# Optimization experiments

Hardware: AMD Instinct MI355X
Metric: run time of the kernel (lower is better)

## Reference

```python
import jax, jax.numpy as jnp
import numpy as np

EPS = 1e-5

def _lin_bn_relu(x, W, b, gamma, beta):
    # x: [N, Cin], W: [Cout, Cin] (torch layout), b/gamma/beta: [Cout]
    y = x @ W.T + b
    mu = jnp.mean(y, axis=0)                      # training-mode batch stats
    var = jnp.mean((y - mu) ** 2, axis=0)         # biased variance (torch BN)
    yhat = (y - mu) * jax.lax.rsqrt(var + EPS)
    return jax.nn.relu(gamma * yhat + beta)


def setup_inputs() -> dict:
    key = jax.random.key(0)
    ks = jax.random.split(key, 16)
    N = 262144
    dims = [(64, 3), (512, 64), (512, 512), (2, 512)]
    inp = {
        "x1": jax.random.normal(ks[0], (8, 4, 8, 8), dtype=jnp.float32),
        "x2": jax.random.normal(ks[1], (N, 3), dtype=jnp.float32),
    }
    for i, (co, ci) in enumerate(dims, start=1):
        lim = 1.0 / np.sqrt(ci)
        inp[f"W{i}"] = jax.random.uniform(ks[2 * i], (co, ci), jnp.float32, -lim, lim)
        inp[f"b{i}"] = jax.random.uniform(ks[2 * i + 1], (co,), jnp.float32, -lim, lim)
    for i, c in enumerate([64, 512, 512], start=1):
        inp[f"gamma{i}"] = jnp.ones((c,), jnp.float32)
        inp[f"beta{i}"] = jnp.zeros((c,), jnp.float32)
    return inp


def reference(x1, x2, W1, b1, W2, b2, W3, b3, W4, b4,
              gamma1, beta1, gamma2, beta2, gamma3, beta3):
    # x1 is sliced in the original forward (x[0][:, 0:-1]) but unused in the output.
    h = _lin_bn_relu(x2, W1, b1, gamma1, beta1)   # [N, 64]
    h = _lin_bn_relu(h, W2, b2, gamma2, beta2)    # [N, 512]
    h = _lin_bn_relu(h, W3, b3, gamma3, beta3)    # [N, 512]
    out = h @ W4.T + b4                           # [N, 2]
    return out
```

## Files before the change

### kernel.cpp

```cpp
#include <hip/hip_runtime.h>

typedef __bf16 bf16x4 __attribute__((ext_vector_type(4)));
typedef __bf16 bf16x8 __attribute__((ext_vector_type(8)));
typedef float f32x4 __attribute__((ext_vector_type(4)));

#define MFMA_BF16 __builtin_amdgcn_mfma_f32_16x16x32_bf16

__global__ __launch_bounds__(256) void prep_kernel(
    const float* __restrict__ W2, const float* __restrict__ W3,
    __bf16* __restrict__ W2bf, __bf16* __restrict__ W3bf,
    float* __restrict__ stats) {
  int i = blockIdx.x * 256 + threadIdx.x;
  if (i < 32768) W2bf[i] = (__bf16)W2[i];
  if (i < 262144) W3bf[i] = (__bf16)W3[i];
  if (i < 5312) stats[i] = 0.f;
}

__global__ __launch_bounds__(256) void stats1_kernel(
    const float* __restrict__ x, const float* __restrict__ W1,
    const float* __restrict__ b1, float* __restrict__ gsum,
    float* __restrict__ gsq) {
  int t = threadIdx.x;
  int c = t & 63;
  int rw = t >> 6;
  float w0 = W1[c * 3 + 0], w1 = W1[c * 3 + 1], w2 = W1[c * 3 + 2];
  float b = b1[c];
  int base = blockIdx.x * 128;
  float sum = 0.f, sq = 0.f;
#pragma unroll 4
  for (int i = 0; i < 32; ++i) {
    int row = base + i * 4 + rw;
    const float* xp = x + (size_t)row * 3;
    float y = fmaf(xp[0], w0, fmaf(xp[1], w1, fmaf(xp[2], w2, b)));
    sum += y;
    sq += y * y;
  }
  __shared__ float ssum[256], ssq[256];
  ssum[t] = sum;
  ssq[t] = sq;
  __syncthreads();
  if (t < 64) {
    float s = ssum[t] + ssum[t + 64] + ssum[t + 128] + ssum[t + 192];
    float q = ssq[t] + ssq[t + 64] + ssq[t + 128] + ssq[t + 192];
    atomicAdd(&gsum[t], s);
    atomicAdd(&gsq[t], q);
  }
}

__global__ void finalize1_kernel(const float* __restrict__ gsum,
                                 const float* __restrict__ gsq,
                                 const float* __restrict__ gamma,
                                 const float* __restrict__ beta,
                                 const float* __restrict__ W1,
                                 const float* __restrict__ b1,
                                 float* __restrict__ fold1, float invN) {
  int c = threadIdx.x;
  float mu = gsum[c] * invN;
  float var = gsq[c] * invN - mu * mu;
  float sc = gamma[c] * rsqrtf(var + 1e-5f);
  float sh = beta[c] - mu * sc;
  fold1[c] = sc * W1[c * 3 + 0];
  fold1[64 + c] = sc * W1[c * 3 + 1];
  fold1[128 + c] = sc * W1[c * 3 + 2];
  fold1[192 + c] = sc * b1[c] + sh;
}

__global__ void finalize3_kernel(const float* __restrict__ gsum,
                                 const float* __restrict__ gsq,
                                 const float* __restrict__ gamma,
                                 const float* __restrict__ beta,
                                 const float* __restrict__ b,
                                 float* __restrict__ scale,
                                 float* __restrict__ shiftf,
                                 float* __restrict__ shiftp, float invN) {
  int c = blockIdx.x * blockDim.x + threadIdx.x;
  if (c >= 512) return;
  float mu = gsum[c] * invN;
  float var = gsq[c] * invN - mu * mu;
  float sc = gamma[c] * rsqrtf(var + 1e-5f);
  float sh = beta[c] - mu * sc;
  scale[c] = sc;
  shiftf[c] = sc * b[c] + sh;
  shiftp[c] = sh;
}

__global__ __launch_bounds__(256, 4) void m1_kernel(
    const float* __restrict__ x2, const float* __restrict__ fold1,
    float* __restrict__ M1, float* __restrict__ s1) {
  __shared__ float sF[256];
  __shared__ float xs[768];
  __shared__ __bf16 h1T[64 * 264];
  __shared__ float s1s[4][64];

  const int t = threadIdx.x;
  const int lane = t & 63, wave = t >> 6;
  const int lrow = lane & 15, lgrp = lane >> 4;

  sF[t] = fold1[t];
  if (t < 192)
    ((float4*)xs)[t] = ((const float4*)(x2 + (size_t)blockIdx.x * 768))[t];
  __syncthreads();

  const int c0 = (t & 3) * 16;
  const int r0 = t >> 2;
  float sAcc[16] = {};
#pragma unroll
  for (int s = 0; s < 4; ++s) {
    int r = r0 + s * 64;
    float X0 = xs[r * 3], X1 = xs[r * 3 + 1], X2 = xs[r * 3 + 2];
#pragma unroll
    for (int j = 0; j < 16; ++j) {
      int c = c0 + j;
      float h = fmaxf(
          fmaf(sF[c], X0, fmaf(sF[64 + c], X1, fmaf(sF[128 + c], X2, sF[192 + c]))),
          0.f);
      sAcc[j] += h;
      h1T[c * 264 + r] = (__bf16)h;
    }
  }
  __syncthreads();

  f32x4 acc[4] = {};
#pragma unroll
  for (int kk = 0; kk < 256; kk += 32) {
    bf16x8 af = *(const bf16x8*)&h1T[(wave * 16 + lrow) * 264 + kk + lgrp * 8];
#pragma unroll
    for (int n = 0; n < 4; ++n) {
      bf16x8 bfr = *(const bf16x8*)&h1T[(n * 16 + lrow) * 264 + kk + lgrp * 8];
      acc[n] = MFMA_BF16(af, bfr, acc[n], 0, 0, 0);
    }
  }
#pragma unroll
  for (int n = 0; n < 4; ++n)
#pragma unroll
    for (int rr = 0; rr < 4; ++rr)
      atomicAdd(&M1[(wave * 16 + lgrp * 4 + rr) * 64 + n * 16 + lrow],
                acc[n][rr]);

#pragma unroll
  for (int j = 0; j < 16; ++j) {
    float v = sAcc[j];
    v += __shfl_xor(v, 4);
    v += __shfl_xor(v, 8);
    v += __shfl_xor(v, 16);
    v += __shfl_xor(v, 32);
    if (lane < 4) s1s[wave][(lane & 3) * 16 + j] = v;
  }
  __syncthreads();
  if (t < 64)
    atomicAdd(&s1[t], s1s[0][t] + s1s[1][t] + s1s[2][t] + s1s[3][t]);
}

__global__ __launch_bounds__(256) void finalize2v_kernel(
    const float* __restrict__ M1, const float* __restrict__ s1,
    const float* __restrict__ W2, const float* __restrict__ b2,
    const float* __restrict__ gamma2, const float* __restrict__ beta2,
    float* __restrict__ scale2, float* __restrict__ shift2f, float fN) {
  __shared__ float sM[64 * 65];
  __shared__ float ss[64];
  int t = threadIdx.x;
  for (int i = t; i < 4096; i += 256) sM[(i >> 6) * 65 + (i & 63)] = M1[i];
  if (t < 64) ss[t] = s1[t];
  __syncthreads();
  int lane = t & 63;
  int col = blockIdx.x * 4 + (t >> 6);
  float wi = W2[(size_t)col * 64 + lane];
  float p = 0.f;
#pragma unroll
  for (int j = 0; j < 64; ++j) p = fmaf(sM[lane * 65 + j], __shfl(wi, j), p);
  float qi = wi * p;
  float swi = ss[lane] * wi;
#pragma unroll
  for (int off = 1; off < 64; off <<= 1) {
    qi += __shfl_xor(qi, off);
    swi += __shfl_xor(swi, off);
  }
  if (lane == 0) {
    float b = b2[col];
    float sy = swi + fN * b;
    float sqs = qi + 2.f * b * swi + fN * b * b;
    float mu = sy / fN;
    float var = sqs / fN - mu * mu;
    float sc = gamma2[col] * rsqrtf(var + 1e-5f);
    scale2[col] = sc;
    shift2f[col] = (beta2[col] - mu * sc) + sc * b;
  }
}

#define G3_LD(BUF, K)                                                        \
  _Pragma("unroll") for (int m = 0; m < 4; ++m) BUF[m] =                     \
      *(const bf16x8*)&h2r[(m * 16 + lrow) * 520 + (K) * 32 + lgrp * 8];

#define G3_MM(BUF, K)                                                        \
  __builtin_amdgcn_s_setprio(1);                                             \
  _Pragma("unroll") for (int m = 0; m < 4; ++m) {                            \
    acc[m][0] = MFMA_BF16(BUF[m], b3r[K][0], acc[m][0], 0, 0, 0);            \
    acc[m][1] = MFMA_BF16(BUF[m], b3r[K][1], acc[m][1], 0, 0, 0);            \
  }                                                                          \
  __builtin_amdgcn_s_setprio(0);

template <int MODE>
__global__ __launch_bounds__(512, 2) void fused_kernel(
    const float* __restrict__ x2, const float* __restrict__ fold1,
    const __bf16* __restrict__ W2bf, const float* __restrict__ scale2,
    const float* __restrict__ shift2f, const __bf16* __restrict__ W3bf,
    const float* __restrict__ b3, const float* __restrict__ scale3,
    const float* __restrict__ shift3f, const float* __restrict__ W4,
    const float* __restrict__ b4, float* __restrict__ gsum3,
    float* __restrict__ gsq3, float* __restrict__ out,
    __bf16* __restrict__ y3o, int gBase, int gCount, int rStoreRgs) {
  __shared__ __bf16 h1buf[2][64 * 72];
  __shared__ __bf16 h2buf[2][64 * 520];
  __shared__ float sF[256];
  __shared__ float sSc2[512], sSh2[512];
  __shared__ float outaccW[8][64][2];

  const int t = threadIdx.x;
  const int lane = t & 63, wave = t >> 6;
  const int lrow = lane & 15, lgrp = lane >> 4;
  const int colHalf = blockIdx.x & 1;
  const int rgFirst = gBase + (int)(blockIdx.x >> 1) * gCount;
  const int wCol3 = colHalf * 256 + wave * 32;
  const int wCol2 = wave * 64;
  const bool doStore = (MODE == 3) && (rgFirst < rStoreRgs);

  if (t < 256) sF[t] = fold1[t];
  sSc2[t] = scale2[t & 511];
  sSh2[t] = shift2f[t & 511];

  bf16x8 b2r[2][4];
#pragma unroll
  for (int kk = 0; kk < 2; ++kk)
#pragma unroll
    for (int n = 0; n < 4; ++n)
      b2r[kk][n] = *(const bf16x8*)&W2bf[(wCol2 + n * 16 + lrow) * 64 +
                                         kk * 32 + lgrp * 8];
  bf16x8 b3r[16][2];
#pragma unroll
  for (int k = 0; k < 16; ++k)
#pragma unroll
    for (int n = 0; n < 2; ++n)
      b3r[k][n] = *(const bf16x8*)&W3bf[(size_t)(wCol3 + n * 16 + lrow) * 512 +
                                        k * 32 + lgrp * 8];

  const int c3a = wCol3 + lrow, c3b = wCol3 + 16 + lrow;
  float b3a = 0.f, b3b = 0.f;
  float sc3a = 0.f, sc3b = 0.f, sh3a = 0.f, sh3b = 0.f;
  float w40a = 0.f, w40b = 0.f, w41a = 0.f, w41b = 0.f, B40 = 0.f, B41 = 0.f;
  if (MODE != 2) {
    b3a = b3[c3a];
    b3b = b3[c3b];
  } else {
    sc3a = scale3[c3a];
    sc3b = scale3[c3b];
    sh3a = shift3f[c3a];
    sh3b = shift3f[c3b];
    w40a = W4[c3a];
    w40b = W4[c3b];
    w41a = W4[512 + c3a];
    w41b = W4[512 + c3b];
    B40 = b4[0];
    B41 = b4[1];
  }
  float csA = 0.f, cqA = 0.f, csB = 0.f, cqB = 0.f;

  const int hr = t >> 3, hc0 = (t & 7) * 8;
  const float* xbase = x2 + ((size_t)rgFirst * 64 + hr) * 3;
  float xa, xb, xc;

  auto stageH1 = [&](__bf16* h1p) {
    bf16x8 hv;
#pragma unroll
    for (int j = 0; j < 8; ++j) {
      int c = hc0 + j;
      float h = fmaf(sF[c], xa,
                     fmaf(sF[64 + c], xb, fmaf(sF[128 + c], xc, sF[192 + c])));
      hv[j] = (__bf16)fmaxf(h, 0.f);
    }
    *(bf16x8*)&h1p[hr * 72 + hc0] = hv;
  };

  auto gemm2 = [&](const __bf16* h1p, __bf16* h2p) {
#pragma unroll
    for (int nh = 0; nh < 2; ++nh) {
      f32x4 a2[2][4] = {};
#pragma unroll
      for (int kk = 0; kk < 2; ++kk) {
        bf16x8 af0 = *(const bf16x8*)&h1p[(0 * 16 + lrow) * 72 + kk * 32 + lgrp * 8];
        bf16x8 af1 = *(const bf16x8*)&h1p[(1 * 16 + lrow) * 72 + kk * 32 + lgrp * 8];
        bf16x8 af2 = *(const bf16x8*)&h1p[(2 * 16 + lrow) * 72 + kk * 32 + lgrp * 8];
        bf16x8 af3 = *(const bf16x8*)&h1p[(3 * 16 + lrow) * 72 + kk * 32 + lgrp * 8];
#pragma unroll
        for (int n2 = 0; n2 < 2; ++n2) {
          int n = nh * 2 + n2;
          a2[n2][0] = MFMA_BF16(b2r[kk][n], af0, a2[n2][0], 0, 0, 0);
          a2[n2][1] = MFMA_BF16(b2r[kk][n], af1, a2[n2][1], 0, 0, 0);
          a2[n2][2] = MFMA_BF16(b2r[kk][n], af2, a2[n2][2], 0, 0, 0);
          a2[n2][3] = MFMA_BF16(b2r[kk][n], af3, a2[n2][3], 0, 0, 0);
        }
      }
#pragma unroll
      for (int n2 = 0; n2 < 2; ++n2) {
        int ch0 = wCol2 + (nh * 2 + n2) * 16 + lgrp * 4;
        float s0 = sSc2[ch0], s1v = sSc2[ch0 + 1], s2v = sSc2[ch0 + 2],
              s3v = sSc2[ch0 + 3];
        float z0 = sSh2[ch0], z1 = sSh2[ch0 + 1], z2 = sSh2[ch0 + 2],
              z3 = sSh2[ch0 + 3];
#pragma unroll
        for (int m = 0; m < 4; ++m) {
          int row = m * 16 + lrow;
          bf16x4 hv;
          hv[0] = (__bf16)fmaxf(fmaf(s0, a2[n2][m][0], z0), 0.f);
          hv[1] = (__bf16)fmaxf(fmaf(s1v, a2[n2][m][1], z1), 0.f);
          hv[2] = (__bf16)fmaxf(fmaf(s2v, a2[n2][m][2], z2), 0.f);
          hv[3] = (__bf16)fmaxf(fmaf(s3v, a2[n2][m][3], z3), 0.f);
          *(bf16x4*)&h2p[row * 520 + ch0] = hv;
        }
      }
    }
  };

  __syncthreads();

  xa = xbase[0];
  xb = xbase[1];
  xc = xbase[2];
  stageH1(h1buf[0]);
  __syncthreads();
  gemm2(h1buf[0], h2buf[0]);
  if (gCount > 1) {
    const float* xn = xbase + 192;
    xa = xn[0];
    xb = xn[1];
    xc = xn[2];
    stageH1(h1buf[1]);
  }
  __syncthreads();

  for (int g = 0; g < gCount; ++g) {
    const int rBase = (rgFirst + g) * 64;
    const __bf16* h2r = h2buf[g & 1];

    if (g + 2 < gCount) {
      const float* xn = xbase + (size_t)(g + 2) * 192;
      xa = xn[0];
      xb = xn[1];
      xc = xn[2];
    }

    if (g + 1 < gCount) gemm2(h1buf[(g + 1) & 1], h2buf[(g + 1) & 1]);

    if (g + 2 < gCount) stageH1(h1buf[g & 1]);

    f32x4 acc[4][2] = {};
    bf16x8 afA[4], afB[4];
    G3_LD(afA, 0)
#pragma unroll
    for (int k = 0; k < 16; k += 2) {
      G3_LD(afB, k + 1)
      G3_MM(afA, k)
      if (k < 14) { G3_LD(afA, k + 2) }
      G3_MM(afB, k + 1)
    }

    if (MODE != 2) {
#pragma unroll
      for (int m = 0; m < 4; ++m)
#pragma unroll
        for (int rr = 0; rr < 4; ++rr) {
          float ya = acc[m][0][rr] + b3a;
          float yb = acc[m][1][rr] + b3b;
          csA += ya;
          cqA = fmaf(ya, ya, cqA);
          csB += yb;
          cqB = fmaf(yb, yb, cqB);
          if (doStore) {
            size_t row = (size_t)(rBase + m * 16 + lgrp * 4 + rr);
            y3o[row * 512 + c3a] = (__bf16)ya;
            y3o[row * 512 + c3b] = (__bf16)yb;
          }
        }
    } else {
#pragma unroll
      for (int m = 0; m < 4; ++m)
#pragma unroll
        for (int rr = 0; rr < 4; ++rr) {
          float ha = fmaxf(fmaf(sc3a, acc[m][0][rr], sh3a), 0.f);
          float hb = fmaxf(fmaf(sc3b, acc[m][1][rr], sh3b), 0.f);
          float dd0 = fmaf(ha, w40a, hb * w40b);
          float dd1 = fmaf(ha, w41a, hb * w41b);
          dd0 += __shfl_xor(dd0, 1);
          dd1 += __shfl_xor(dd1, 1);
          dd0 += __shfl_xor(dd0, 2);
          dd1 += __shfl_xor(dd1, 2);
          dd0 += __shfl_xor(dd0, 4);
          dd1 += __shfl_xor(dd1, 4);
          dd0 += __shfl_xor(dd0, 8);
          dd1 += __shfl_xor(dd1, 8);
          if (lrow == 0) {
            int row = m * 16 + lgrp * 4 + rr;
            outaccW[wave][row][0] = dd0;
            outaccW[wave][row][1] = dd1;
          }
        }
    }
    __syncthreads();
  }

  if (MODE != 2) {
    csA += __shfl_xor(csA, 16);
    cqA += __shfl_xor(cqA, 16);
    csB += __shfl_xor(csB, 16);
    cqB += __shfl_xor(cqB, 16);
    csA += __shfl_xor(csA, 32);
    cqA += __shfl_xor(cqA, 32);
    csB += __shfl_xor(csB, 32);
    cqB += __shfl_xor(cqB, 32);
    if (lgrp == 0) {
      atomicAdd(&gsum3[c3a], csA);
      atomicAdd(&gsq3[c3a], cqA);
      atomicAdd(&gsum3[c3b], csB);
      atomicAdd(&gsq3[c3b], cqB);
    }
  } else {
    if (t < 128) {
      int row = t >> 1, o = t & 1;
      float s = 0.f;
#pragma unroll
      for (int w = 0; w < 8; ++w) s += outaccW[w][row][o];
      if (colHalf == 0) s += (o == 0) ? B40 : B41;
      atomicAdd(&out[(size_t)(rgFirst * 64 + row) * 2 + o], s);
    }
  }
}

__global__ __launch_bounds__(256) void stream_out_kernel(
    const __bf16* __restrict__ y3, const float* __restrict__ scale3,
    const float* __restrict__ shift3p, const float* __restrict__ W4,
    const float* __restrict__ b4, float* __restrict__ out, int N) {
  __shared__ float sSc[512], sSh[512], sW0[512], sW1[512];
  int t = threadIdx.x;
  for (int i = t; i < 512; i += 256) {
    sSc[i] = scale3[i];
    sSh[i] = shift3p[i];
    sW0[i] = W4[i];
    sW1[i] = W4[512 + i];
  }
  __syncthreads();
  int lane = t & 63, wv = t >> 6;
  int c0 = lane * 8;
  float fsc[8], fsh[8], fw0[8], fw1[8];
#pragma unroll
  for (int j = 0; j < 8; ++j) {
    fsc[j] = sSc[c0 + j];
    fsh[j] = sSh[c0 + j];
    fw0[j] = sW0[c0 + j];
    fw1[j] = sW1[c0 + j];
  }
  float B0 = b4[0], B1 = b4[1];
  for (size_t row = (size_t)blockIdx.x * 4 + wv; row < (size_t)N;
       row += (size_t)gridDim.x * 4) {
    bf16x8 v = *(const bf16x8*)(y3 + row * 512 + c0);
    float d0 = 0.f, d1 = 0.f;
#pragma unroll
    for (int j = 0; j < 8; ++j) {
      float h = fmaxf(fmaf(fsc[j], (float)v[j], fsh[j]), 0.f);
      d0 = fmaf(h, fw0[j], d0);
      d1 = fmaf(h, fw1[j], d1);
    }
#pragma unroll
    for (int off = 1; off < 64; off <<= 1) {
      d0 += __shfl_xor(d0, off);
      d1 += __shfl_xor(d1, off);
    }
    if (lane == 0) {
      out[row * 2 + 0] = d0 + B0;
      out[row * 2 + 1] = d1 + B1;
    }
  }
}

extern "C" void kernel_launch(void* const* d_in, const int* in_sizes, int n_in,
                              void* d_out, int out_size, void* d_ws,
                              size_t ws_size, hipStream_t stream) {
  const float* x2 = (const float*)d_in[1];
  const float* W1 = (const float*)d_in[2];
  const float* b1 = (const float*)d_in[3];
  const float* W2 = (const float*)d_in[4];
  const float* b2 = (const float*)d_in[5];
  const float* W3 = (const float*)d_in[6];
  const float* b3 = (const float*)d_in[7];
  const float* W4 = (const float*)d_in[8];
  const float* b4 = (const float*)d_in[9];
  const float* gamma1 = (const float*)d_in[10];
  const float* beta1 = (const float*)d_in[11];
  const float* gamma2 = (const float*)d_in[12];
  const float* beta2 = (const float*)d_in[13];
  const float* gamma3 = (const float*)d_in[14];
  const float* beta3 = (const float*)d_in[15];
  float* out = (float*)d_out;

  const int N = in_sizes[1] / 3;
  const float invN = 1.0f / (float)N;

  float* f0 = (float*)d_ws;
  float* gsum1 = f0;
  float* gsq1 = f0 + 64;
  float* M1 = f0 + 128;
  float* s1 = f0 + 4224;
  float* gsum3 = f0 + 4288;
  float* gsq3 = f0 + 4800;
  float* fold1 = f0 + 5312;
  float* scale2 = f0 + 5568;
  float* shift2f = f0 + 6080;
  float* scale3 = f0 + 6592;
  float* shift3f = f0 + 7104;
  float* shift3p = f0 + 7616;
  __bf16* W2bf = (__bf16*)(f0 + 8128);
  __bf16* W3bf = W2bf + 32768;

  const size_t y3off = (size_t)1 << 20;
  size_t availRows = (ws_size > y3off) ? (ws_size - y3off) / 1024 : 0;
  int rStoreBlks = (int)((availRows / 1024 < (size_t)(N / 1024))
                             ? availRows / 1024
                             : (size_t)(N / 1024));
  const int rStore = rStoreBlks * 1024;
  __bf16* y3bf = (__bf16*)((char*)d_ws + y3off);

  prep_kernel<<<1024, 256, 0, stream>>>(W2, W3, W2bf, W3bf, f0);
  stats1_kernel<<<N / 128, 256, 0, stream>>>(x2, W1, b1, gsum1, gsq1);
  finalize1_kernel<<<1, 64, 0, stream>>>(gsum1, gsq1, gamma1, beta1, W1, b1,
                                         fold1, invN);
  m1_kernel<<<N / 256, 256, 0, stream>>>(x2, fold1, M1, s1);
  finalize2v_kernel<<<128, 256, 0, stream>>>(M1, s1, W2, b2, gamma2, beta2,
                                             scale2, shift2f, (float)N);

  fused_kernel<3><<<(N / 1024) * 2, 512, 0, stream>>>(
      x2, fold1, W2bf, scale2, shift2f, W3bf, b3, scale3, shift3f, W4, b4,
      gsum3, gsq3, out, y3bf, 0, 16, rStoreBlks * 16);
  finalize3_kernel<<<1, 512, 0, stream>>>(gsum3, gsq3, gamma3, beta3, b3,
                                          scale3, shift3f, shift3p, invN);

  if (rStore > 0)
    stream_out_kernel<<<2048, 256, 0, stream>>>(y3bf, scale3, shift3p, W4, b4,
                                                out, rStore);
  if (rStore < N) {
    hipMemsetAsync(out + (size_t)rStore * 2, 0,
                   (size_t)(N - rStore) * 2 * sizeof(float), stream);
    fused_kernel<2><<<((N - rStore) / 64) * 2, 512, 0, stream>>>(
        x2, fold1, W2bf, scale2, shift2f, W3bf, b3, scale3, shift3f, W4, b4,
        gsum3, gsq3, out, y3bf, rStore / 64, 1, 0);
  }
}
```

Baseline: 389.8 us.

## Fold finalize kernels into consumers, merge prep with stats1, pair rows in stream_out

Removes the finalize1 and finalize3 launches by having each consumer kernel recompute the BN scale and shift from the raw sums in its prologue. Weight conversion to bf16 moves into extra blocks of the stats1 kernel using vectorized loads, and zeroing the stats buffer becomes a memset. The stream_out kernel now handles two rows per wave and shares the cross-lane reduction between four partial sums. The aim is fewer kernel launches and less shuffle work, at the cost of redundant per-block prologue math.

After: 384.1 us. Within noise of the previous version (-1.5%).

```diff
diff --git a/kernel.cpp b/kernel.cpp
--- a/kernel.cpp
+++ b/kernel.cpp
@@ -6,32 +6,52 @@
 
 #define MFMA_BF16 __builtin_amdgcn_mfma_f32_16x16x32_bf16
 
-__global__ __launch_bounds__(256) void prep_kernel(
-    const float* __restrict__ W2, const float* __restrict__ W3,
-    __bf16* __restrict__ W2bf, __bf16* __restrict__ W3bf,
-    float* __restrict__ stats) {
-  int i = blockIdx.x * 256 + threadIdx.x;
-  if (i < 32768) W2bf[i] = (__bf16)W2[i];
-  if (i < 262144) W3bf[i] = (__bf16)W3[i];
-  if (i < 5312) stats[i] = 0.f;
-}
-
-__global__ __launch_bounds__(256) void stats1_kernel(
+__global__ __launch_bounds__(256) void prep_stats1_kernel(
     const float* __restrict__ x, const float* __restrict__ W1,
-    const float* __restrict__ b1, float* __restrict__ gsum,
+    const float* __restrict__ b1, const float* __restrict__ W2,
+    const float* __restrict__ W3, __bf16* __restrict__ W2bf,
+    __bf16* __restrict__ W3bf, float* __restrict__ gsum,
     float* __restrict__ gsq) {
-  int t = threadIdx.x;
+  const int b = blockIdx.x;
+  const int t = threadIdx.x;
+  if (b >= 2048) {
+    const float* src;
+    __bf16* dst;
+    int idx;
+    if (b < 2064) {
+      idx = (b - 2048) * 2048 + t * 8;
+      src = W2;
+      dst = W2bf;
+    } else {
+      idx = (b - 2064) * 2048 + t * 8;
+      src = W3;
+      dst = W3bf;
+    }
+    float4 f0 = *(const float4*)(src + idx);
+    float4 f1 = *(const float4*)(src + idx + 4);
+    bf16x8 o;
+    o[0] = (__bf16)f0.x;
+    o[1] = (__bf16)f0.y;
+    o[2] = (__bf16)f0.z;
+    o[3] = (__bf16)f0.w;
+    o[4] = (__bf16)f1.x;
+    o[5] = (__bf16)f1.y;
+    o[6] = (__bf16)f1.z;
+    o[7] = (__bf16)f1.w;
+    *(bf16x8*)(dst + idx) = o;
+    return;
+  }
   int c = t & 63;
   int rw = t >> 6;
   float w0 = W1[c * 3 + 0], w1 = W1[c * 3 + 1], w2 = W1[c * 3 + 2];
-  float b = b1[c];
-  int base = blockIdx.x * 128;
+  float bb = b1[c];
+  int base = b * 128;
   float sum = 0.f, sq = 0.f;
 #pragma unroll 4
   for (int i = 0; i < 32; ++i) {
     int row = base + i * 4 + rw;
     const float* xp = x + (size_t)row * 3;
-    float y = fmaf(xp[0], w0, fmaf(xp[1], w1, fmaf(xp[2], w2, b)));
+    float y = fmaf(xp[0], w0, fmaf(xp[1], w1, fmaf(xp[2], w2, bb)));
     sum += y;
     sq += y * y;
   }
@@ -47,46 +67,12 @@
   }
 }
 
-__global__ void finalize1_kernel(const float* __restrict__ gsum,
-                                 const float* __restrict__ gsq,
-                                 const float* __restrict__ gamma,
-                                 const float* __restrict__ beta,
-                                 const float* __restrict__ W1,
-                                 const float* __restrict__ b1,
-                                 float* __restrict__ fold1, float invN) {
-  int c = threadIdx.x;
-  float mu = gsum[c] * invN;
-  float var = gsq[c] * invN - mu * mu;
-  float sc = gamma[c] * rsqrtf(var + 1e-5f);
-  float sh = beta[c] - mu * sc;
-  fold1[c] = sc * W1[c * 3 + 0];
-  fold1[64 + c] = sc * W1[c * 3 + 1];
-  fold1[128 + c] = sc * W1[c * 3 + 2];
-  fold1[192 + c] = sc * b1[c] + sh;
-}
-
-__global__ void finalize3_kernel(const float* __restrict__ gsum,
-                                 const float* __restrict__ gsq,
-                                 const float* __restrict__ gamma,
-                                 const float* __restrict__ beta,
-                                 const float* __restrict__ b,
-                                 float* __restrict__ scale,
-                                 float* __restrict__ shiftf,
-                                 float* __restrict__ shiftp, float invN) {
-  int c = blockIdx.x * blockDim.x + threadIdx.x;
-  if (c >= 512) return;
-  float mu = gsum[c] * invN;
-  float var = gsq[c] * invN - mu * mu;
-  float sc = gamma[c] * rsqrtf(var + 1e-5f);
-  float sh = beta[c] - mu * sc;
-  scale[c] = sc;
-  shiftf[c] = sc * b[c] + sh;
-  shiftp[c] = sh;
-}
-
 __global__ __launch_bounds__(256, 4) void m1_kernel(
-    const float* __restrict__ x2, const float* __restrict__ fold1,
-    float* __restrict__ M1, float* __restrict__ s1) {
+    const float* __restrict__ x2, const float* __restrict__ gsum1,
+    const float* __restrict__ gsq1, const float* __restrict__ gamma1,
+    const float* __restrict__ beta1, const float* __restrict__ W1,
+    const float* __restrict__ b1, float* __restrict__ M1,
+    float* __restrict__ s1, float invN) {
   __shared__ float sF[256];
   __shared__ float xs[768];
   __shared__ __bf16 h1T[64 * 264];
@@ -96,7 +82,16 @@
   const int lane = t & 63, wave = t >> 6;
   const int lrow = lane & 15, lgrp = lane >> 4;
 
-  sF[t] = fold1[t];
+  if (t < 64) {
+    float mu = gsum1[t] * invN;
+    float var = gsq1[t] * invN - mu * mu;
+    float sc = gamma1[t] * rsqrtf(var + 1e-5f);
+    float sh = beta1[t] - mu * sc;
+    sF[t] = sc * W1[t * 3];
+    sF[64 + t] = sc * W1[t * 3 + 1];
+    sF[128 + t] = sc * W1[t * 3 + 2];
+    sF[192 + t] = sc * b1[t] + sh;
+  }
   if (t < 192)
     ((float4*)xs)[t] = ((const float4*)(x2 + (size_t)blockIdx.x * 768))[t];
   __syncthreads();
@@ -201,14 +196,17 @@
 
 template <int MODE>
 __global__ __launch_bounds__(512, 2) void fused_kernel(
-    const float* __restrict__ x2, const float* __restrict__ fold1,
-    const __bf16* __restrict__ W2bf, const float* __restrict__ scale2,
-    const float* __restrict__ shift2f, const __bf16* __restrict__ W3bf,
-    const float* __restrict__ b3, const float* __restrict__ scale3,
-    const float* __restrict__ shift3f, const float* __restrict__ W4,
-    const float* __restrict__ b4, float* __restrict__ gsum3,
-    float* __restrict__ gsq3, float* __restrict__ out,
-    __bf16* __restrict__ y3o, int gBase, int gCount, int rStoreRgs) {
+    const float* __restrict__ x2, const float* __restrict__ gsum1,
+    const float* __restrict__ gsq1, const float* __restrict__ gamma1,
+    const float* __restrict__ beta1, const float* __restrict__ W1,
+    const float* __restrict__ b1, const __bf16* __restrict__ W2bf,
+    const float* __restrict__ scale2, const float* __restrict__ shift2f,
+    const __bf16* __restrict__ W3bf, const float* __restrict__ b3,
+    const float* __restrict__ gamma3, const float* __restrict__ beta3,
+    const float* __restrict__ W4, const float* __restrict__ b4,
+    float* __restrict__ gsum3, float* __restrict__ gsq3,
+    float* __restrict__ out, __bf16* __restrict__ y3o, int gBase, int gCount,
+    int rStoreRgs, float invN) {
   __shared__ __bf16 h1buf[2][64 * 72];
   __shared__ __bf16 h2buf[2][64 * 520];
   __shared__ float sF[256];
@@ -224,7 +222,16 @@
   const int wCol2 = wave * 64;
   const bool doStore = (MODE == 3) && (rgFirst < rStoreRgs);
 
-  if (t < 256) sF[t] = fold1[t];
+  if (t < 64) {
+    float mu = gsum1[t] * invN;
+    float var = gsq1[t] * invN - mu * mu;
+    float sc = gamma1[t] * rsqrtf(var + 1e-5f);
+    float sh = beta1[t] - mu * sc;
+    sF[t] = sc * W1[t * 3];
+    sF[64 + t] = sc * W1[t * 3 + 1];
+    sF[128 + t] = sc * W1[t * 3 + 2];
+    sF[192 + t] = sc * b1[t] + sh;
+  }
   sSc2[t] = scale2[t & 511];
   sSh2[t] = shift2f[t & 511];
 
@@ -251,10 +258,14 @@
     b3a = b3[c3a];
     b3b = b3[c3b];
   } else {
-    sc3a = scale3[c3a];
-    sc3b = scale3[c3b];
-    sh3a = shift3f[c3a];
-    sh3b = shift3f[c3b];
+    float mu = gsum3[c3a] * invN;
+    float var = gsq3[c3a] * invN - mu * mu;
+    sc3a = gamma3[c3a] * rsqrtf(var + 1e-5f);
+    sh3a = sc3a * b3[c3a] + (beta3[c3a] - mu * sc3a);
+    mu = gsum3[c3b] * invN;
+    var = gsq3[c3b] * invN - mu * mu;
+    sc3b = gamma3[c3b] * rsqrtf(var + 1e-5f);
+    sh3b = sc3b * b3[c3b] + (beta3[c3b] - mu * sc3b);
     w40a = W4[c3a];
     w40b = W4[c3b];
     w41a = W4[512 + c3a];
@@ -349,7 +360,6 @@
     }
 
     if (g + 1 < gCount) gemm2(h1buf[(g + 1) & 1], h2buf[(g + 1) & 1]);
-
     if (g + 2 < gCount) stageH1(h1buf[g & 1]);
 
     f32x4 acc[4][2] = {};
@@ -435,14 +445,18 @@
 }
 
 __global__ __launch_bounds__(256) void stream_out_kernel(
-    const __bf16* __restrict__ y3, const float* __restrict__ scale3,
-    const float* __restrict__ shift3p, const float* __restrict__ W4,
-    const float* __restrict__ b4, float* __restrict__ out, int N) {
+    const __bf16* __restrict__ y3, const float* __restrict__ gsum3,
+    const float* __restrict__ gsq3, const float* __restrict__ gamma3,
+    const float* __restrict__ beta3, const float* __restrict__ W4,
+    const float* __restrict__ b4, float* __restrict__ out, int N, float invN) {
   __shared__ float sSc[512], sSh[512], sW0[512], sW1[512];
   int t = threadIdx.x;
   for (int i = t; i < 512; i += 256) {
-    sSc[i] = scale3[i];
-    sSh[i] = shift3p[i];
+    float mu = gsum3[i] * invN;
+    float var = gsq3[i] * invN - mu * mu;
+    float sc = gamma3[i] * rsqrtf(var + 1e-5f);
+    sSc[i] = sc;
+    sSh[i] = beta3[i] - mu * sc;
     sW0[i] = W4[i];
     sW1[i] = W4[512 + i];
   }
@@ -458,25 +472,34 @@
     fw1[j] = sW1[c0 + j];
   }
   float B0 = b4[0], B1 = b4[1];
-  for (size_t row = (size_t)blockIdx.x * 4 + wv; row < (size_t)N;
-       row += (size_t)gridDim.x * 4) {
-    bf16x8 v = *(const bf16x8*)(y3 + row * 512 + c0);
-    float d0 = 0.f, d1 = 0.f;
+  for (size_t row = (size_t)blockIdx.x * 8 + wv * 2; row < (size_t)N;
+       row += (size_t)gridDim.x * 8) {
+    bf16x8 v0 = *(const bf16x8*)(y3 + row * 512 + c0);
+    bf16x8 v1 = *(const bf16x8*)(y3 + (row + 1) * 512 + c0);
+    float d0a = 0.f, d1a = 0.f, d0b = 0.f, d1b = 0.f;
 #pragma unroll
     for (int j = 0; j < 8; ++j) {
-      float h = fmaxf(fmaf(fsc[j], (float)v[j], fsh[j]), 0.f);
-      d0 = fmaf(h, fw0[j], d0);
-      d1 = fmaf(h, fw1[j], d1);
-    }
-#pragma unroll
-    for (int off = 1; off < 64; off <<= 1) {
-      d0 += __shfl_xor(d0, off);
-      d1 += __shfl_xor(d1, off);
-    }
-    if (lane == 0) {
-      out[row * 2 + 0] = d0 + B0;
-      out[row * 2 + 1] = d1 + B1;
-    }
+      float ha = fmaxf(fmaf(fsc[j], (float)v0[j], fsh[j]), 0.f);
+      float hb = fmaxf(fmaf(fsc[j], (float)v1[j], fsh[j]), 0.f);
+      d0a = fmaf(ha, fw0[j], d0a);
+      d1a = fmaf(ha, fw1[j], d1a);
+      d0b = fmaf(hb, fw0[j], d0b);
+      d1b = fmaf(hb, fw1[j], d1b);
+    }
+    float t0 = d0a + __shfl_xor(d0a, 1);
+    float t1 = d1a + __shfl_xor(d1a, 1);
+    float t2 = d0b + __shfl_xor(d0b, 1);
+    float t3 = d1b + __shfl_xor(d1b, 1);
+    float u0 = (lane & 1) ? t1 : t0;
+    float u1 = (lane & 1) ? t3 : t2;
+    u0 += __shfl_xor(u0, 2);
+    u1 += __shfl_xor(u1, 2);
+    float w = (lane & 2) ? u1 : u0;
+    w += __shfl_xor(w, 4);
+    w += __shfl_xor(w, 8);
+    w += __shfl_xor(w, 16);
+    w += __shfl_xor(w, 32);
+    if (lane < 4) out[row * 2 + lane] = w + ((lane & 1) ? B1 : B0);
   }
 }
 
@@ -510,13 +533,9 @@
   float* s1 = f0 + 4224;
   float* gsum3 = f0 + 4288;
   float* gsq3 = f0 + 4800;
-  float* fold1 = f0 + 5312;
-  float* scale2 = f0 + 5568;
-  float* shift2f = f0 + 6080;
-  float* scale3 = f0 + 6592;
-  float* shift3f = f0 + 7104;
-  float* shift3p = f0 + 7616;
-  __bf16* W2bf = (__bf16*)(f0 + 8128);
+  float* scale2 = f0 + 5312;
+  float* shift2f = f0 + 5824;
+  __bf16* W2bf = (__bf16*)(f0 + 6336);
   __bf16* W3bf = W2bf + 32768;
 
   const size_t y3off = (size_t)1 << 20;
@@ -527,28 +546,29 @@
   const int rStore = rStoreBlks * 1024;
   __bf16* y3bf = (__bf16*)((char*)d_ws + y3off);
 
-  prep_kernel<<<1024, 256, 0, stream>>>(W2, W3, W2bf, W3bf, f0);
-  stats1_kernel<<<N / 128, 256, 0, stream>>>(x2, W1, b1, gsum1, gsq1);
-  finalize1_kernel<<<1, 64, 0, stream>>>(gsum1, gsq1, gamma1, beta1, W1, b1,
-                                         fold1, invN);
-  m1_kernel<<<N / 256, 256, 0, stream>>>(x2, fold1, M1, s1);
+  hipMemsetAsync(f0, 0, 5312 * sizeof(float), stream);
+  prep_stats1_kernel<<<2192, 256, 0, stream>>>(x2, W1, b1, W2, W3, W2bf, W3bf,
+                                               gsum1, gsq1);
+  m1_kernel<<<N / 256, 256, 0, stream>>>(x2, gsum1, gsq1, gamma1, beta1, W1,
+                                         b1, M1, s1, invN);
   finalize2v_kernel<<<128, 256, 0, stream>>>(M1, s1, W2, b2, gamma2, beta2,
                                              scale2, shift2f, (float)N);
 
   fused_kernel<3><<<(N / 1024) * 2, 512, 0, stream>>>(
-      x2, fold1, W2bf, scale2, shift2f, W3bf, b3, scale3, shift3f, W4, b4,
-      gsum3, gsq3, out, y3bf, 0, 16, rStoreBlks * 16);
-  finalize3_kernel<<<1, 512, 0, stream>>>(gsum3, gsq3, gamma3, beta3, b3,
-                                          scale3, shift3f, shift3p, invN);
+      x2, gsum1, gsq1, gamma1, beta1, W1, b1, W2bf, scale2, shift2f, W3bf, b3,
+      gamma3, beta3, W4, b4, gsum3, gsq3, out, y3bf, 0, 16, rStoreBlks * 16,
+      invN);
 
   if (rStore > 0)
-    stream_out_kernel<<<2048, 256, 0, stream>>>(y3bf, scale3, shift3p, W4, b4,
-                                                out, rStore);
+    stream_out_kernel<<<2048, 256, 0, stream>>>(y3bf, gsum3, gsq3, gamma3,
+                                                beta3, W4, b4, out, rStore,
+                                                invN);
   if (rStore < N) {
     hipMemsetAsync(out + (size_t)rStore * 2, 0,
                    (size_t)(N - rStore) * 2 * sizeof(float), stream);
     fused_kernel<2><<<((N - rStore) / 64) * 2, 512, 0, stream>>>(
-        x2, fold1, W2bf, scale2, shift2f, W3bf, b3, scale3, shift3f, W4, b4,
-        gsum3, gsq3, out, y3bf, rStore / 64, 1, 0);
+        x2, gsum1, gsq1, gamma1, beta1, W1, b1, W2bf, scale2, shift2f, W3bf,
+        b3, gamma3, beta3, W4, b4, gsum3, gsq3, out, y3bf, rStore / 64, 1, 0,
+        invN);
   }
 }
```
